# Optimization experiments

Measured on AMD Instinct MI355X. Metric: run time of the kernel, lower is better.

Reference implementation:

```python
import jax, jax.numpy as jnp
import numpy as np

N_HEAD = 16
ROPE_BASE = 10000.0


def rope_cos_sin(T, head_dim, dtype):
    inv_freq = 1.0 / (ROPE_BASE ** (jnp.arange(0, head_dim, 2, dtype=jnp.float32) / head_dim))
    t = jnp.arange(T, dtype=jnp.float32)
    freqs = jnp.einsum('i,j->ij', t, inv_freq)          # [T, head_dim/2]
    emb = jnp.concatenate([freqs, freqs], axis=-1)       # [T, head_dim]
    return jnp.cos(emb).astype(dtype), jnp.sin(emb).astype(dtype)


def rotate_half(x):
    h = x.shape[-1] // 2
    return jnp.concatenate([-x[..., h:], x[..., :h]], axis=-1)


def setup_inputs() -> dict:
    key = jax.random.key(0)
    ks = jax.random.split(key, 5)
    B, T, C = 2, 1024, 2048
    s = 0.02
    return {
        'x': jax.random.normal(ks[0], (B, T, C), dtype=jnp.float32),
        'Wq': jax.random.normal(ks[1], (C, C), dtype=jnp.float32) * s,
        'Wk': jax.random.normal(ks[2], (C, C), dtype=jnp.float32) * s,
        'Wv': jax.random.normal(ks[3], (C, C), dtype=jnp.float32) * s,
        'Wo': jax.random.normal(ks[4], (C, C), dtype=jnp.float32) * s,
    }


def reference(x, Wq, Wk, Wv, Wo):
    B, T, C = x.shape
    H = N_HEAD
    D = C // H
    # torch Linear: y = x @ W.T  (W is [out, in])
    q = jnp.einsum('btc,oc->bto', x, Wq).reshape(B, T, H, D).transpose(0, 2, 1, 3)
    k = jnp.einsum('btc,oc->bto', x, Wk).reshape(B, T, H, D).transpose(0, 2, 1, 3)
    v = jnp.einsum('btc,oc->bto', x, Wv).reshape(B, T, H, D).transpose(0, 2, 1, 3)
    cos, sin = rope_cos_sin(T, D, x.dtype)               # [T, D]
    cos = cos[None, None]                                 # [1,1,T,D]
    sin = sin[None, None]
    q = q * cos + rotate_half(q) * sin
    k = k * cos + rotate_half(k) * sin
    scale = 1.0 / jnp.sqrt(jnp.asarray(D, dtype=x.dtype))
    att = jnp.einsum('bhqd,bhkd->bhqk', q, k) * scale    # [B,H,T,T]
    causal = jnp.tril(jnp.ones((T, T), dtype=bool))
    att = jnp.where(causal[None, None], att, jnp.finfo(x.dtype).min)
    att = jax.nn.softmax(att, axis=-1)
    y = jnp.einsum('bhqk,bhkd->bhqd', att, v)            # [B,H,T,D]
    y = y.transpose(0, 2, 1, 3).reshape(B, T, C)
    return jnp.einsum('btc,oc->bto', y, Wo)
```

## Files before the change

kernel.cpp:

```cpp
#include <hip/hip_runtime.h>
#include <stdint.h>

typedef unsigned short u16;
typedef __bf16 bf16x8 __attribute__((ext_vector_type(8)));
typedef float  f32x4  __attribute__((ext_vector_type(4)));

#define B_  2
#define T_  1024
#define C_  2048
#define H_  16
#define D_  128
#define NTENS 4194304

__device__ __forceinline__ u16 f2bf(float f) {
    union { float f; uint32_t u; } v; v.f = f;
    uint32_t r = (v.u + 0x7FFFu + ((v.u >> 16) & 1u)) >> 16;
    return (u16)r;
}
__device__ __forceinline__ float bf2f(u16 h) {
    union { uint32_t u; float f; } v; v.u = ((uint32_t)h) << 16;
    return v.f;
}

__global__ __launch_bounds__(256) void k_convert(
    const float* __restrict__ x, const float* __restrict__ wq,
    const float* __restrict__ wk, const float* __restrict__ wv,
    const float* __restrict__ wo, u16* __restrict__ dst)
{
    int z = blockIdx.z;
    const float* src = (z == 0) ? x : (z == 1) ? wq : (z == 2) ? wk : (z == 3) ? wv : wo;
    u16* d = dst + (size_t)z * NTENS;
    size_t i = ((size_t)blockIdx.x * 256 + threadIdx.x) * 4;
    float4 v = *(const float4*)(src + i);
    ushort4 o;
    o.x = f2bf(v.x); o.y = f2bf(v.y); o.z = f2bf(v.z); o.w = f2bf(v.w);
    *(ushort4*)(d + i) = o;
}

__global__ void k_rope_table(float* __restrict__ ct, float* __restrict__ st)
{
    int t = blockIdx.x, d = threadIdx.x;
    float inv = expf(-(float)d * (9.210340371976184f / 64.0f));
    float th = (float)t * inv;
    float s, c;
    sincosf(th, &s, &c);
    ct[t * 64 + d] = c;
    st[t * 64 + d] = s;
}

__global__ __launch_bounds__(256) void k_rope(
    u16* __restrict__ q, u16* __restrict__ k,
    const float* __restrict__ ct, const float* __restrict__ st)
{
    int idx = blockIdx.x * 256 + threadIdx.x;
    int d = idx & 63;
    int h = (idx >> 6) & 15;
    int t = (idx >> 10) & 1023;
    int b = idx >> 20;
    size_t base = ((size_t)(b * T_ + t)) * C_ + h * D_ + d;
    float c = ct[t * 64 + d], s = st[t * 64 + d];
    const float sc = 0.08838834764831845f;
    float q0 = bf2f(q[base]), q1 = bf2f(q[base + 64]);
    q[base]      = f2bf((q0 * c - q1 * s) * sc);
    q[base + 64] = f2bf((q1 * c + q0 * s) * sc);
    float k0 = bf2f(k[base]), k1 = bf2f(k[base + 64]);
    k[base]      = f2bf(k0 * c - k1 * s);
    k[base + 64] = f2bf(k1 * c + k0 * s);
}

template<typename OutT>
__device__ __forceinline__ void gemm_tile_nt(
    const u16* __restrict__ A, int lda,
    const u16* __restrict__ Bp, int ldb,
    OutT* __restrict__ Cp, int ldc,
    int m0, int n0, int K, float scale,
    u16* As, u16* Bs)
{
    const int tid  = threadIdx.x;
    const int wave = tid >> 6;
    const int lane = tid & 63;
    const int wc   = wave << 5;
    const int frow = lane & 15;
    const int quad = lane >> 4;

    const int lrow8  = lane >> 3;
    const int slot   = lane & 7;
    const int gchunk = slot ^ lrow8;

    f32x4 acc[4][2] = {};

    size_t aoff[2], boff[4];
#pragma unroll
    for (int i = 0; i < 2; ++i) {
        int r = (i << 5) + (wave << 3) + lrow8;
        aoff[i] = (size_t)(m0 + r) * lda + (gchunk << 3);
    }
#pragma unroll
    for (int i = 0; i < 4; ++i) {
        int r = (i << 5) + (wave << 3) + lrow8;
        boff[i] = (size_t)(n0 + r) * ldb + (gchunk << 3);
    }

    for (int kt = 0; kt < K; kt += 64) {
#pragma unroll
        for (int i = 0; i < 2; ++i) {
            int c = (i << 2) + wave;
            __builtin_amdgcn_global_load_lds(
                (const __attribute__((address_space(1))) void*)(A + aoff[i] + kt),
                (__attribute__((address_space(3))) void*)(As + (c << 9)), 16, 0, 0);
        }
#pragma unroll
        for (int i = 0; i < 4; ++i) {
            int c = (i << 2) + wave;
            __builtin_amdgcn_global_load_lds(
                (const __attribute__((address_space(1))) void*)(Bp + boff[i] + kt),
                (__attribute__((address_space(3))) void*)(Bs + (c << 9)), 16, 0, 0);
        }
        __syncthreads();

#pragma unroll
        for (int ks = 0; ks < 2; ++ks) {
            int lk = (ks << 2) + quad;
            bf16x8 af[4], bfv[2];
#pragma unroll
            for (int i = 0; i < 4; ++i) {
                int ar = (i << 4) + frow;
                af[i] = *(const bf16x8*)&As[ar * 64 + ((lk ^ (frow & 7)) << 3)];
            }
#pragma unroll
            for (int j = 0; j < 2; ++j) {
                int br = wc + (j << 4) + frow;
                bfv[j] = *(const bf16x8*)&Bs[br * 64 + ((lk ^ (frow & 7)) << 3)];
            }
#pragma unroll
            for (int i = 0; i < 4; ++i)
#pragma unroll
                for (int j = 0; j < 2; ++j)
                    acc[i][j] = __builtin_amdgcn_mfma_f32_16x16x32_bf16(
                        af[i], bfv[j], acc[i][j], 0, 0, 0);
        }
        __syncthreads();
    }

#pragma unroll
    for (int i = 0; i < 4; ++i)
#pragma unroll
        for (int j = 0; j < 2; ++j)
#pragma unroll
            for (int r = 0; r < 4; ++r) {
                int m = m0 + (i << 4) + (quad << 2) + r;
                int n = n0 + wc + (j << 4) + frow;
                float val = acc[i][j][r] * scale;
                if constexpr (sizeof(OutT) == 2)
                    Cp[(size_t)m * ldc + n] = f2bf(val);
                else
                    Cp[(size_t)m * ldc + n] = val;
            }
}

__global__ __launch_bounds__(256) void k_gemm_qkv(
    const u16* __restrict__ xb, const u16* __restrict__ wq,
    const u16* __restrict__ wk, const u16* __restrict__ wv,
    u16* __restrict__ q, u16* __restrict__ k, u16* __restrict__ v)
{
    __shared__ u16 As[64 * 64], Bs[128 * 64];
    int z = blockIdx.z;
    const u16* Bp = (z == 0) ? wq : (z == 1) ? wk : wv;
    u16* Op       = (z == 0) ? q  : (z == 1) ? k  : v;
    gemm_tile_nt<u16>(xb, C_, Bp, C_, Op, C_,
                      blockIdx.y * 64, blockIdx.x * 128, C_, 1.0f, As, Bs);
}

__global__ __launch_bounds__(256) void k_flash(
    const u16* __restrict__ qb, const u16* __restrict__ kb,
    const u16* __restrict__ vb, u16* __restrict__ yb)
{
    __shared__ u16 Qs[64 * 128];
    __shared__ u16 Ks[64 * 128];
    __shared__ u16 Vs[128 * 72];

    const int bx  = blockIdx.x;
    const int bh  = bx & 31, b = bh >> 4, h = bh & 15;
    const int qt  = 15 - (bx >> 5);
    const int tid = threadIdx.x, wave = tid >> 6, lane = tid & 63;
    const int frow = lane & 15, quad = lane >> 4;

    const u16* qbase = qb + (size_t)b * (T_ * C_) + h * D_;
    const u16* kbase = kb + (size_t)b * (T_ * C_) + h * D_;
    const u16* vbase = vb + (size_t)b * (T_ * C_) + h * D_;
    const int q0 = qt << 6;

    {
        const int r4 = lane >> 4, s16 = lane & 15;
#pragma unroll
        for (int i = 0; i < 4; ++i) {
            int c = (i << 2) + wave;
            int row = (c << 2) + r4;
            int g = (s16 & 8) | ((s16 & 7) ^ (row & 7));
            __builtin_amdgcn_global_load_lds(
                (const __attribute__((address_space(1))) void*)(qbase + (size_t)(q0 + row) * C_ + (g << 3)),
                (__attribute__((address_space(3))) void*)(Qs + (c << 9)), 16, 0, 0);
        }
    }

    f32x4 Y[8] = {};
    float mrow[4], lrow[4];
#pragma unroll
    for (int r = 0; r < 4; ++r) { mrow[r] = -3e38f; lrow[r] = 0.f; }

    const int tok = q0 + wave * 16 + quad * 4;

    for (int kt = 0; kt <= qt; ++kt) {
        const int k0 = kt << 6;
        {
            const int r4 = lane >> 4, s16 = lane & 15;
#pragma unroll
            for (int i = 0; i < 4; ++i) {
                int c = (i << 2) + wave;
                int row = (c << 2) + r4;
                int g = (s16 & 8) | ((s16 & 7) ^ (row & 7));
                __builtin_amdgcn_global_load_lds(
                    (const __attribute__((address_space(1))) void*)(kbase + (size_t)(k0 + row) * C_ + (g << 3)),
                    (__attribute__((address_space(3))) void*)(Ks + (c << 9)), 16, 0, 0);
            }
        }
        {
#pragma unroll
            for (int i = 0; i < 4; ++i) {
                int idx = (i << 8) + tid;
                int kr = idx & 63;
                int n8 = (idx >> 6) << 3;
                uint4 vv = *(const uint4*)&vbase[(size_t)(k0 + kr) * C_ + n8];
                u16 tmp[8];
                *(uint4*)tmp = vv;
#pragma unroll
                for (int e = 0; e < 8; ++e)
                    Vs[(n8 + e) * 72 + kr] = tmp[e];
            }
        }
        __syncthreads();

        f32x4 S[4] = {};
#pragma unroll
        for (int ks = 0; ks < 4; ++ks) {
            int lk = (ks << 2) + quad;
            int sw = ((lk & 8) | ((lk & 7) ^ (frow & 7))) << 3;
            bf16x8 a = *(const bf16x8*)&Qs[(wave * 16 + frow) * 128 + sw];
#pragma unroll
            for (int jj = 0; jj < 4; ++jj) {
                bf16x8 bb = *(const bf16x8*)&Ks[((jj << 4) + frow) * 128 + sw];
                S[jj] = __builtin_amdgcn_mfma_f32_16x16x32_bf16(a, bb, S[jj], 0, 0, 0);
            }
        }

        if (kt == qt) {
#pragma unroll
            for (int jj = 0; jj < 4; ++jj) {
                int colg = k0 + (jj << 4) + frow;
#pragma unroll
                for (int r = 0; r < 4; ++r)
                    if (colg > tok + r) S[jj][r] = -1e30f;
            }
        }

        float al[4];
#pragma unroll
        for (int r = 0; r < 4; ++r) {
            float tm = fmaxf(fmaxf(S[0][r], S[1][r]), fmaxf(S[2][r], S[3][r]));
#pragma unroll
            for (int off = 8; off > 0; off >>= 1) tm = fmaxf(tm, __shfl_xor(tm, off));
            float mn = fmaxf(mrow[r], tm);
            al[r] = __expf(mrow[r] - mn);
            mrow[r] = mn;
            float rs = 0.f;
#pragma unroll
            for (int jj = 0; jj < 4; ++jj) {
                float e = __expf(S[jj][r] - mn);
                S[jj][r] = e;
                rs += e;
            }
#pragma unroll
            for (int off = 8; off > 0; off >>= 1) rs += __shfl_xor(rs, off);
            lrow[r] = lrow[r] * al[r] + rs;
        }
#pragma unroll
        for (int dj = 0; dj < 8; ++dj)
#pragma unroll
            for (int r = 0; r < 4; ++r) Y[dj][r] *= al[r];

        __syncthreads();

        u16* Ps = Ks;
#pragma unroll
        for (int jj = 0; jj < 4; ++jj)
#pragma unroll
            for (int r = 0; r < 4; ++r)
                Ps[(wave * 16 + quad * 4 + r) * 72 + (jj << 4) + frow] = f2bf(S[jj][r]);

#pragma unroll
        for (int ks = 0; ks < 2; ++ks) {
            bf16x8 pa = *(const bf16x8*)&Ps[(wave * 16 + frow) * 72 + (ks << 5) + (quad << 3)];
#pragma unroll
            for (int dj = 0; dj < 8; ++dj) {
                bf16x8 vv = *(const bf16x8*)&Vs[((dj << 4) + frow) * 72 + (ks << 5) + (quad << 3)];
                Y[dj] = __builtin_amdgcn_mfma_f32_16x16x32_bf16(pa, vv, Y[dj], 0, 0, 0);
            }
        }
        __syncthreads();
    }

    u16* ybase = yb + (size_t)b * (T_ * C_) + h * D_;
#pragma unroll
    for (int r = 0; r < 4; ++r) {
        float inv = 1.0f / lrow[r];
#pragma unroll
        for (int dj = 0; dj < 8; ++dj)
            ybase[(size_t)(tok + r) * C_ + (dj << 4) + frow] = f2bf(Y[dj][r] * inv);
    }
}

__global__ __launch_bounds__(256) void k_gemm_out(
    const u16* __restrict__ yb, const u16* __restrict__ wo, float* __restrict__ out)
{
    __shared__ u16 As[64 * 64], Bs[128 * 64];
    gemm_tile_nt<float>(yb, C_, wo, C_, out, C_,
                        blockIdx.y * 64, blockIdx.x * 128, C_, 1.0f, As, Bs);
}

extern "C" void kernel_launch(void* const* d_in, const int* in_sizes, int n_in,
                              void* d_out, int out_size, void* d_ws, size_t ws_size,
                              hipStream_t stream)
{
    (void)in_sizes; (void)n_in; (void)out_size; (void)ws_size;
    const float* x  = (const float*)d_in[0];
    const float* Wq = (const float*)d_in[1];
    const float* Wk = (const float*)d_in[2];
    const float* Wv = (const float*)d_in[3];
    const float* Wo = (const float*)d_in[4];

    u16* ws  = (u16*)d_ws;
    u16* xb  = ws;
    u16* wqb = ws + (size_t)1 * NTENS;
    u16* wkb = ws + (size_t)2 * NTENS;
    u16* wvb = ws + (size_t)3 * NTENS;
    u16* wob = ws + (size_t)4 * NTENS;
    u16* qb  = ws + (size_t)5 * NTENS;
    u16* kb  = ws + (size_t)6 * NTENS;
    u16* vb  = ws + (size_t)7 * NTENS;
    u16* yb  = ws + (size_t)8 * NTENS;
    float* ct = (float*)(ws + (size_t)9 * NTENS);
    float* st = ct + 65536;

    k_convert   <<<dim3(4096, 1, 5), 256, 0, stream>>>(x, Wq, Wk, Wv, Wo, ws);
    k_rope_table<<<dim3(1024), 64, 0, stream>>>(ct, st);
    k_gemm_qkv  <<<dim3(16, 32, 3), 256, 0, stream>>>(xb, wqb, wkb, wvb, qb, kb, vb);
    k_rope      <<<dim3(8192), 256, 0, stream>>>(qb, kb, ct, st);
    k_flash     <<<dim3(512), 256, 0, stream>>>(qb, kb, vb, yb);
    k_gemm_out  <<<dim3(16, 32, 1), 256, 0, stream>>>(yb, wob, (float*)d_out);
}
```

Before: 272.9 us.

## Fuse RoPE into QKV GEMM epilogue, rebalance flash order, shrink out-GEMM tile

Removes the separate RoPE kernel by applying rotary embedding and the query scale in the QKV GEMM epilogue. The tile is staged through shared memory so each thread holds both halves of a head. The flash kernel's query-tile order is changed so the second half of blocks runs short tiles first, which is meant to balance the causal workload across CUs. The output GEMM uses a 32-row M tile, doubling block count to improve occupancy on the 256-CU device. The cost is extra LDS traffic and a barrier in the epilogue.

```diff
diff --git a/kernel.cpp b/kernel.cpp
--- a/kernel.cpp
+++ b/kernel.cpp
@@ -48,34 +48,19 @@
     st[t * 64 + d] = s;
 }
 
-__global__ __launch_bounds__(256) void k_rope(
-    u16* __restrict__ q, u16* __restrict__ k,
-    const float* __restrict__ ct, const float* __restrict__ st)
-{
-    int idx = blockIdx.x * 256 + threadIdx.x;
-    int d = idx & 63;
-    int h = (idx >> 6) & 15;
-    int t = (idx >> 10) & 1023;
-    int b = idx >> 20;
-    size_t base = ((size_t)(b * T_ + t)) * C_ + h * D_ + d;
-    float c = ct[t * 64 + d], s = st[t * 64 + d];
-    const float sc = 0.08838834764831845f;
-    float q0 = bf2f(q[base]), q1 = bf2f(q[base + 64]);
-    q[base]      = f2bf((q0 * c - q1 * s) * sc);
-    q[base + 64] = f2bf((q1 * c + q0 * s) * sc);
-    float k0 = bf2f(k[base]), k1 = bf2f(k[base + 64]);
-    k[base]      = f2bf(k0 * c - k1 * s);
-    k[base + 64] = f2bf(k1 * c + k0 * s);
-}
-
-template<typename OutT>
+template<int MTILE, int EPI>
 __device__ __forceinline__ void gemm_tile_nt(
     const u16* __restrict__ A, int lda,
     const u16* __restrict__ Bp, int ldb,
-    OutT* __restrict__ Cp, int ldc,
-    int m0, int n0, int K, float scale,
-    u16* As, u16* Bs)
-{
+    void* __restrict__ Cp, int ldc,
+    int m0, int n0, int K,
+    u16* SMEM, const float* __restrict__ ct, const float* __restrict__ st, int z)
+{
+    constexpr int MF  = MTILE / 16;
+    constexpr int ACH = MTILE / 32;
+    u16* As = SMEM;
+    u16* Bs = SMEM + MTILE * 64;
+
     const int tid  = threadIdx.x;
     const int wave = tid >> 6;
     const int lane = tid & 63;
@@ -87,12 +72,13 @@
     const int slot   = lane & 7;
     const int gchunk = slot ^ lrow8;
 
-    f32x4 acc[4][2] = {};
-
-    size_t aoff[2], boff[4];
-#pragma unroll
-    for (int i = 0; i < 2; ++i) {
-        int r = (i << 5) + (wave << 3) + lrow8;
+    f32x4 acc[MF][2] = {};
+
+    size_t aoff[ACH], boff[4];
+#pragma unroll
+    for (int i = 0; i < ACH; ++i) {
+        int c = (i << 2) + wave;
+        int r = (c << 3) + lrow8;
         aoff[i] = (size_t)(m0 + r) * lda + (gchunk << 3);
     }
 #pragma unroll
@@ -103,7 +89,7 @@
 
     for (int kt = 0; kt < K; kt += 64) {
 #pragma unroll
-        for (int i = 0; i < 2; ++i) {
+        for (int i = 0; i < ACH; ++i) {
             int c = (i << 2) + wave;
             __builtin_amdgcn_global_load_lds(
                 (const __attribute__((address_space(1))) void*)(A + aoff[i] + kt),
@@ -121,9 +107,9 @@
 #pragma unroll
         for (int ks = 0; ks < 2; ++ks) {
             int lk = (ks << 2) + quad;
-            bf16x8 af[4], bfv[2];
-#pragma unroll
-            for (int i = 0; i < 4; ++i) {
+            bf16x8 af[MF], bfv[2];
+#pragma unroll
+            for (int i = 0; i < MF; ++i) {
                 int ar = (i << 4) + frow;
                 af[i] = *(const bf16x8*)&As[ar * 64 + ((lk ^ (frow & 7)) << 3)];
             }
@@ -133,7 +119,7 @@
                 bfv[j] = *(const bf16x8*)&Bs[br * 64 + ((lk ^ (frow & 7)) << 3)];
             }
 #pragma unroll
-            for (int i = 0; i < 4; ++i)
+            for (int i = 0; i < MF; ++i)
 #pragma unroll
                 for (int j = 0; j < 2; ++j)
                     acc[i][j] = __builtin_amdgcn_mfma_f32_16x16x32_bf16(
@@ -142,33 +128,91 @@
         __syncthreads();
     }
 
-#pragma unroll
-    for (int i = 0; i < 4; ++i)
+    if constexpr (EPI == 2) {
+        if (z < 2) {
+            u16* L = SMEM;
+#pragma unroll
+            for (int i = 0; i < MF; ++i)
+#pragma unroll
+                for (int j = 0; j < 2; ++j)
+#pragma unroll
+                    for (int r = 0; r < 4; ++r) {
+                        int rl = (i << 4) + (quad << 2) + r;
+                        int d  = wc + (j << 4) + frow;
+                        L[rl * 136 + d] = f2bf(acc[i][j][r]);
+                    }
+            __syncthreads();
+
+            int rl = tid >> 2;
+            int d0 = (tid & 3) << 4;
+            int t  = (m0 + rl) & 1023;
+            uint4 lo4[2], hi4[2];
+            lo4[0] = *(const uint4*)&L[rl * 136 + d0];
+            lo4[1] = *(const uint4*)&L[rl * 136 + d0 + 8];
+            hi4[0] = *(const uint4*)&L[rl * 136 + 64 + d0];
+            hi4[1] = *(const uint4*)&L[rl * 136 + 64 + d0 + 8];
+            const u16* lo = (const u16*)lo4;
+            const u16* hi = (const u16*)hi4;
+            float sc = (z == 0) ? 0.08838834764831845f : 1.0f;
+            u16 o0[16], o1[16];
+            const float* ctp = ct + t * 64 + d0;
+            const float* stp = st + t * 64 + d0;
+#pragma unroll
+            for (int e = 0; e < 16; ++e) {
+                float c = ctp[e], s = stp[e];
+                float a = bf2f(lo[e]), b = bf2f(hi[e]);
+                o0[e] = f2bf((a * c - b * s) * sc);
+                o1[e] = f2bf((b * c + a * s) * sc);
+            }
+            u16* Op = (u16*)Cp;
+            size_t rbase = (size_t)(m0 + rl) * ldc + n0;
+            *(uint4*)&Op[rbase + d0]          = ((uint4*)o0)[0];
+            *(uint4*)&Op[rbase + d0 + 8]      = ((uint4*)o0)[1];
+            *(uint4*)&Op[rbase + 64 + d0]     = ((uint4*)o1)[0];
+            *(uint4*)&Op[rbase + 64 + d0 + 8] = ((uint4*)o1)[1];
+            return;
+        }
+        u16* Op = (u16*)Cp;
+#pragma unroll
+        for (int i = 0; i < MF; ++i)
+#pragma unroll
+            for (int j = 0; j < 2; ++j)
+#pragma unroll
+                for (int r = 0; r < 4; ++r) {
+                    int m = m0 + (i << 4) + (quad << 2) + r;
+                    int n = n0 + wc + (j << 4) + frow;
+                    Op[(size_t)m * ldc + n] = f2bf(acc[i][j][r]);
+                }
+        return;
+    }
+
+#pragma unroll
+    for (int i = 0; i < MF; ++i)
 #pragma unroll
         for (int j = 0; j < 2; ++j)
 #pragma unroll
             for (int r = 0; r < 4; ++r) {
                 int m = m0 + (i << 4) + (quad << 2) + r;
                 int n = n0 + wc + (j << 4) + frow;
-                float val = acc[i][j][r] * scale;
-                if constexpr (sizeof(OutT) == 2)
-                    Cp[(size_t)m * ldc + n] = f2bf(val);
+                if constexpr (EPI == 1)
+                    ((u16*)Cp)[(size_t)m * ldc + n] = f2bf(acc[i][j][r]);
                 else
-                    Cp[(size_t)m * ldc + n] = val;
+                    ((float*)Cp)[(size_t)m * ldc + n] = acc[i][j][r];
             }
 }
 
 __global__ __launch_bounds__(256) void k_gemm_qkv(
     const u16* __restrict__ xb, const u16* __restrict__ wq,
     const u16* __restrict__ wk, const u16* __restrict__ wv,
-    u16* __restrict__ q, u16* __restrict__ k, u16* __restrict__ v)
-{
-    __shared__ u16 As[64 * 64], Bs[128 * 64];
+    u16* __restrict__ q, u16* __restrict__ k, u16* __restrict__ v,
+    const float* __restrict__ ct, const float* __restrict__ st)
+{
+    __shared__ u16 SMEM[64 * 64 + 128 * 64];
     int z = blockIdx.z;
     const u16* Bp = (z == 0) ? wq : (z == 1) ? wk : wv;
     u16* Op       = (z == 0) ? q  : (z == 1) ? k  : v;
-    gemm_tile_nt<u16>(xb, C_, Bp, C_, Op, C_,
-                      blockIdx.y * 64, blockIdx.x * 128, C_, 1.0f, As, Bs);
+    gemm_tile_nt<64, 2>(xb, C_, Bp, C_, Op, C_,
+                        blockIdx.y * 64, blockIdx.x * 128, C_, SMEM, ct, st, z);
 }
 
 __global__ __launch_bounds__(256) void k_flash(
@@ -181,7 +225,7 @@
 
     const int bx  = blockIdx.x;
     const int bh  = bx & 31, b = bh >> 4, h = bh & 15;
-    const int qt  = 15 - (bx >> 5);
+    const int qt  = (bx < 256) ? (15 - (bx >> 5)) : ((bx >> 5) - 8);
     const int tid = threadIdx.x, wave = tid >> 6, lane = tid & 63;
     const int frow = lane & 15, quad = lane >> 4;
 
@@ -322,9 +366,9 @@
 __global__ __launch_bounds__(256) void k_gemm_out(
     const u16* __restrict__ yb, const u16* __restrict__ wo, float* __restrict__ out)
 {
-    __shared__ u16 As[64 * 64], Bs[128 * 64];
-    gemm_tile_nt<float>(yb, C_, wo, C_, out, C_,
-                        blockIdx.y * 64, blockIdx.x * 128, C_, 1.0f, As, Bs);
+    __shared__ u16 SMEM[32 * 64 + 128 * 64];
+    gemm_tile_nt<32, 0>(yb, C_, wo, C_, out, C_,
+                        blockIdx.y * 32, blockIdx.x * 128, C_, SMEM, nullptr, nullptr, 0);
 }
 
 extern "C" void kernel_launch(void* const* d_in, const int* in_sizes, int n_in,
@@ -353,8 +397,7 @@
 
     k_convert   <<<dim3(4096, 1, 5), 256, 0, stream>>>(x, Wq, Wk, Wv, Wo, ws);
     k_rope_table<<<dim3(1024), 64, 0, stream>>>(ct, st);
-    k_gemm_qkv  <<<dim3(16, 32, 3), 256, 0, stream>>>(xb, wqb, wkb, wvb, qb, kb, vb);
-    k_rope      <<<dim3(8192), 256, 0, stream>>>(qb, kb, ct, st);
+    k_gemm_qkv  <<<dim3(16, 32, 3), 256, 0, stream>>>(xb, wqb, wkb, wvb, qb, kb, vb, ct, st);
     k_flash     <<<dim3(512), 256, 0, stream>>>(qb, kb, vb, yb);
-    k_gemm_out  <<<dim3(16, 32, 1), 256, 0, stream>>>(yb, wob, (float*)d_out);
-}
+    k_gemm_out  <<<dim3(16, 64, 1), 256, 0, stream>>>(yb, wob, (float*)d_out);
+}
```

Result: no change. 271.3 us (-0.6%).
